# Performance work log

Measured on AMD Instinct MI355X. Metric: run time of the kernel, lower is better.

The kernel has to match this reference:

```python
import jax, jax.numpy as jnp
import numpy as np

D_MODEL = 512
N_HEAD = 8
D_HEAD = 64
N_LAYER = 4
D_INNER = 2048
IN_CH = 2048
N_CLS = 64
B, T = 2, 2048
LN_EPS = 1e-5


def layer_norm(x, s, b):
    mu = jnp.mean(x, axis=-1, keepdims=True)
    var = jnp.mean(jnp.square(x - mu), axis=-1, keepdims=True)
    return (x - mu) * jax.lax.rsqrt(var + LN_EPS) * s + b


def rel_shift(x):
    # x: [q, k, b, n] -> Transformer-XL relative shift
    q, k, b, n = x.shape
    zp = jnp.zeros((q, 1, b, n), x.dtype)
    x = jnp.concatenate([zp, x], axis=1)          # [q, k+1, b, n]
    x = x.reshape(k + 1, q, b, n)[1:]             # drop first row
    return x.reshape(q, k, b, n)


def setup_inputs() -> dict:
    key = jax.random.key(0)
    ks = jax.random.split(key, 12)
    s = 0.02
    return {
        "x": jax.random.normal(ks[0], (B, IN_CH, T), jnp.float32),
        "emb_w": jax.random.normal(ks[1], (D_MODEL, IN_CH), jnp.float32) * s,
        "emb_b": jnp.zeros((D_MODEL,), jnp.float32),
        "r_w_bias": jax.random.normal(ks[2], (N_HEAD, D_HEAD), jnp.float32) * s,
        "r_r_bias": jax.random.normal(ks[3], (N_HEAD, D_HEAD), jnp.float32) * s,
        "qkv_w": jax.random.normal(ks[4], (N_LAYER, 3 * N_HEAD * D_HEAD, D_MODEL), jnp.float32) * s,
        "qkv_b": jnp.zeros((N_LAYER, 3 * N_HEAD * D_HEAD), jnp.float32),
        "r_proj_w": jax.random.normal(ks[5], (N_LAYER, N_HEAD * D_HEAD, D_MODEL), jnp.float32) * s,
        "o_w": jax.random.normal(ks[6], (N_LAYER, D_MODEL, N_HEAD * D_HEAD), jnp.float32) * s,
        "ln1_s": jnp.ones((N_LAYER, D_MODEL), jnp.float32),
        "ln1_b": jnp.zeros((N_LAYER, D_MODEL), jnp.float32),
        "ff1_w": jax.random.normal(ks[7], (N_LAYER, D_INNER, D_MODEL), jnp.float32) * s,
        "ff1_b": jnp.zeros((N_LAYER, D_INNER), jnp.float32),
        "ff2_w": jax.random.normal(ks[8], (N_LAYER, D_MODEL, D_INNER), jnp.float32) * s,
        "ff2_b": jnp.zeros((N_LAYER, D_MODEL), jnp.float32),
        "ln2_s": jnp.ones((N_LAYER, D_MODEL), jnp.float32),
        "ln2_b": jnp.zeros((N_LAYER, D_MODEL), jnp.float32),
        "cls_w": jax.random.normal(ks[9], (N_CLS, D_MODEL), jnp.float32) * s,
        "cls_b": jnp.zeros((N_CLS,), jnp.float32),
    }


def reference(x, emb_w, emb_b, r_w_bias, r_r_bias, qkv_w, qkv_b, r_proj_w, o_w,
              ln1_s, ln1_b, ff1_w, ff1_b, ff2_w, ff2_b, ln2_s, ln2_b, cls_w, cls_b):
    b, _, t = x.shape
    d = D_MODEL
    # 1x1 conv embedding, then to [T, B, d_model] layout as in _forward
    h = jnp.einsum('dc,bct->tbd', emb_w, x) + emb_b

    # sinusoidal positional embedding over pos_seq = klen-1 .. 0 (klen == qlen, mem_len=0)
    pos_seq = jnp.arange(t - 1, -1, -1, dtype=h.dtype)
    inv_freq = 1.0 / (10000.0 ** (jnp.arange(0, d, 2, dtype=h.dtype) / d))
    sinusoid = pos_seq[:, None] * inv_freq[None, :]
    pos_emb = jnp.concatenate([jnp.sin(sinusoid), jnp.cos(sinusoid)], axis=-1)  # [T, d]

    scale = 1.0 / (D_HEAD ** 0.5)
    for i in range(N_LAYER):
        w = h
        heads = jnp.einsum('ed,tbd->tbe', qkv_w[i], w) + qkv_b[i]          # [T,B,3*H*Dh]
        q, k, v = jnp.split(heads, 3, axis=-1)
        q = q.reshape(t, b, N_HEAD, D_HEAD)
        k = k.reshape(t, b, N_HEAD, D_HEAD)
        v = v.reshape(t, b, N_HEAD, D_HEAD)
        r_head_k = jnp.einsum('ed,td->te', r_proj_w[i], pos_emb).reshape(t, N_HEAD, D_HEAD)

        AC = jnp.einsum('ibnd,jbnd->ijbn', q + r_w_bias, k)                # content term
        BD = rel_shift(jnp.einsum('ibnd,jnd->ijbn', q + r_r_bias, r_head_k))  # position term
        attn_prob = jax.nn.softmax((AC + BD) * scale, axis=1)              # softmax over keys
        attn_vec = jnp.einsum('ijbn,jbnd->ibnd', attn_prob, v).reshape(t, b, N_HEAD * D_HEAD)
        attn_out = jnp.einsum('de,tbe->tbd', o_w[i], attn_vec)             # o_net (no bias)
        h = layer_norm(w + attn_out, ln1_s[i], ln1_b[i])                   # post-lnorm

        ff = jnp.einsum('fd,tbd->tbf', ff1_w[i], h) + ff1_b[i]
        ff = jax.nn.relu(ff)
        ff = jnp.einsum('df,tbf->tbd', ff2_w[i], ff) + ff2_b[i]
        h = layer_norm(h + ff, ln2_s[i], ln2_b[i])

    # 1x1 conv classifier -> [B, num_classes, T]
    out = jnp.einsum('kd,tbd->bkt', cls_w, h) + cls_b[None, :, None]
    return out
```

## Files before the change

kernel.cpp:

```cpp
#include <hip/hip_runtime.h>
#include <hip/hip_bf16.h>
#include <math.h>


#define T_   2048
#define B_   2
#define DM   512
#define NH   8
#define DH   64
#define DI   2048
#define INCH 2048
#define NCLS 64
#define MT   4096

typedef __attribute__((ext_vector_type(8))) short short8;
typedef __attribute__((ext_vector_type(4))) float float4v;

#define QSCALE 0.1803368801111204f

__device__ inline ushort f2bf(float f) {
  uint u = __float_as_uint(f);
  return (ushort)((u + 0x7FFFu + ((u >> 16) & 1u)) >> 16);
}
__device__ inline float bf2f(ushort h) { return __uint_as_float(((uint)h) << 16); }
__device__ inline uint pkbf(float a, float b) {
  __hip_bfloat162 h = __float22bfloat162_rn(float2{a, b});
  return *(uint*)&h;
}
__device__ inline void gload16(const void* g, void* lds) {
  __builtin_amdgcn_global_load_lds(
      (const __attribute__((address_space(1))) void*)g,
      (__attribute__((address_space(3))) void*)lds, 16, 0, 0);
}

__global__ __launch_bounds__(256) void pos_kernel(ushort* __restrict__ pe) {
  int idx = blockIdx.x * 256 + threadIdx.x;
  if (idx >= T_ * DM) return;
  int t = idx >> 9;
  int i = idx & 511;
  int j = (i < 256) ? i : (i - 256);
  float invf = __builtin_amdgcn_exp2f((float)(-2 * j) * 0.025952563241307517f);
  float a = (float)(T_ - 1 - t) * invf;
  pe[idx] = f2bf((i < 256) ? sinf(a) : cosf(a));
}

__global__ __launch_bounds__(256) void cvt6_kernel(
    const float* s0, ushort* d0, int n0,
    const float* s1, ushort* d1, int n1,
    const float* s2, ushort* d2, int n2,
    const float* s3, ushort* d3, int n3,
    const float* s4, ushort* d4, int n4,
    const float* s5, ushort* d5, int n5)
{
  const float* s; ushort* d; int n;
  switch (blockIdx.y) {
    case 0: s = s0; d = d0; n = n0; break;
    case 1: s = s1; d = d1; n = n1; break;
    case 2: s = s2; d = d2; n = n2; break;
    case 3: s = s3; d = d3; n = n3; break;
    case 4: s = s4; d = d4; n = n4; break;
    default: s = s5; d = d5; n = n5; break;
  }
  int i = blockIdx.x * 256 + threadIdx.x;
  if (i >= n) return;
  float4 v = ((const float4*)s)[i];
  ushort4 w = { f2bf(v.x), f2bf(v.y), f2bf(v.z), f2bf(v.w) };
  ((ushort4*)d)[i] = w;
}

__global__ __launch_bounds__(256) void clsw_cvt_kernel(const float* __restrict__ w,
                                                       ushort* __restrict__ wb) {
  int i = blockIdx.x * 256 + threadIdx.x;
  ushort4 o;
  if (i < 8192) {
    float4 v = ((const float4*)w)[i];
    o = ushort4{ f2bf(v.x), f2bf(v.y), f2bf(v.z), f2bf(v.w) };
  } else {
    o = ushort4{ 0, 0, 0, 0 };
  }
  ((ushort4*)wb)[i] = o;
}

__global__ __launch_bounds__(256) void xpose_kernel(const float* __restrict__ x,
                                                    ushort* __restrict__ xb) {
  __shared__ float s[32][33];
  int t0 = blockIdx.x * 32, k0 = blockIdx.y * 32, b = blockIdx.z;
  int tx = threadIdx.x & 31, ty = threadIdx.x >> 5;
#pragma unroll
  for (int l = 0; l < 4; ++l) {
    int k = k0 + ty + l * 8;
    s[ty + l * 8][tx] = x[((size_t)b * INCH + k) * T_ + t0 + tx];
  }
  __syncthreads();
#pragma unroll
  for (int l = 0; l < 4; ++l) {
    int t = t0 + ty + l * 8;
    xb[((size_t)(t * 2 + b)) * INCH + k0 + tx] = f2bf(s[tx][ty + l * 8]);
  }
}

template<int TM, int OUTMODE, bool RELU>
__global__ __launch_bounds__(256) void gemm_bf16(
    const ushort* __restrict__ A, const ushort* __restrict__ W,
    const float* __restrict__ bias, float* __restrict__ Cf, ushort* __restrict__ Cb,
    int M, int N, int K)
{
  __shared__ __attribute__((aligned(16))) ushort As[TM * 64];
  __shared__ __attribute__((aligned(16))) ushort Bs[128 * 64];
  const int NI = TM / 32;
  const int tid  = threadIdx.x;
  const int wave = tid >> 6, lane = tid & 63;
  const int quad = lane >> 4, lidx = lane & 15;
  const int m0 = blockIdx.y * TM, n0 = blockIdx.x * 128;
  const int r8 = lane >> 3;
  const int cs = ((lane & 7) ^ (r8 & 7)) * 8;

  float4v acc[NI * 4];
#pragma unroll
  for (int i = 0; i < NI * 4; ++i) acc[i] = (float4v){0.f, 0.f, 0.f, 0.f};

  const int wm = (wave >> 1) * (TM / 2), wn = (wave & 1) * 64;

  for (int k0 = 0; k0 < K; k0 += 64) {
    __syncthreads();
#pragma unroll
    for (int g = 0; g < TM / 32; ++g) {
      int r0 = wave * 8 + g * 32;
      gload16(A + (size_t)(m0 + r0 + r8) * K + k0 + cs, &As[r0 * 64]);
    }
#pragma unroll
    for (int g = 0; g < 4; ++g) {
      int r0 = wave * 8 + g * 32;
      gload16(W + (size_t)(n0 + r0 + r8) * K + k0 + cs, &Bs[r0 * 64]);
    }
    __syncthreads();

#pragma unroll
    for (int kb = 0; kb < 2; ++kb) {
      short8 af[NI], bf4[4];
      const int ch = (((kb * 4 + quad) ^ (lidx & 7)) * 8);
#pragma unroll
      for (int i = 0; i < NI; ++i)
        af[i] = *(const short8*)&As[(wm + i * 16 + lidx) * 64 + ch];
#pragma unroll
      for (int j = 0; j < 4; ++j)
        bf4[j] = *(const short8*)&Bs[(wn + j * 16 + lidx) * 64 + ch];
#pragma unroll
      for (int i = 0; i < NI; ++i)
#pragma unroll
        for (int j = 0; j < 4; ++j)
          acc[i * 4 + j] = __builtin_amdgcn_mfma_f32_16x16x32_bf16(af[i], bf4[j], acc[i * 4 + j], 0, 0, 0);
    }
  }

  float bj[4];
#pragma unroll
  for (int j = 0; j < 4; ++j) bj[j] = bias ? bias[n0 + wn + j * 16 + lidx] : 0.f;

  if (OUTMODE == 3 && n0 >= 1024) {
    ushort* vt = (ushort*)Cf;
    __syncthreads();
#pragma unroll
    for (int i = 0; i < NI; ++i)
#pragma unroll
      for (int j = 0; j < 4; ++j)
#pragma unroll
        for (int reg = 0; reg < 4; ++reg) {
          int c2 = wn + j * 16 + lidx;
          int rl = wm + i * 16 + quad * 4 + reg;
          float v = acc[i * 4 + j][reg] + bj[j];
          ushort* buf = (c2 < 64) ? As : Bs;
          buf[(c2 & 63) * 128 + (rl ^ ((c2 & 7) << 4))] = f2bf(v);
        }
    __syncthreads();
    const int t0g = m0 >> 1;
    const int low = tid & 15, b2 = low & 1, tb = low >> 1;
#pragma unroll
    for (int s = 0; s < 8; ++s) {
      int dd = s * 16 + (tid >> 4);
      const ushort* buf = (dd < 64) ? As : Bs;
      ushort tmp[8];
#pragma unroll
      for (int q2 = 0; q2 < 8; ++q2) {
        int rl = (tb * 8 + q2) * 2 + b2;
        tmp[q2] = buf[(dd & 63) * 128 + (rl ^ ((dd & 7) << 4))];
      }
      int dg = n0 + dd - 1024;
      int n2h = dg >> 6, ddd = dg & 63;
      *(uint4*)&vt[((size_t)((b2 * 8 + n2h) * 64 + ddd)) * (size_t)T_ + t0g + tb * 8] = *(uint4*)tmp;
    }
  } else {
#pragma unroll
    for (int i = 0; i < NI; ++i) {
      int rbase = m0 + wm + i * 16 + quad * 4;
#pragma unroll
      for (int j = 0; j < 4; ++j) {
        int col = n0 + wn + j * 16 + lidx;
#pragma unroll
        for (int reg = 0; reg < 4; ++reg) {
          float v = acc[i * 4 + j][reg] + bj[j];
          if (RELU) v = fmaxf(v, 0.f);
          size_t off = (size_t)(rbase + reg) * N + col;
          if (OUTMODE == 0 || OUTMODE == 2) Cf[off] = v;
          if (OUTMODE != 0) Cb[off] = f2bf(v);
        }
      }
    }
  }
}

#define GT 68

__device__ inline short8 bfrag(const char* base, int lidx, int quad, int kb) {
  return *(const short8*)(base + lidx * 128 + ((((kb << 2) + quad) ^ (lidx & 7)) << 4));
}

__global__ __launch_bounds__(256, 3) void attn_mfma_kernel(
    const ushort* __restrict__ heads, const ushort* __restrict__ rk,
    const ushort* __restrict__ vtg,
    const float* __restrict__ rwb, const float* __restrict__ rrb,
    float* __restrict__ O0, float* __restrict__ O1, float* __restrict__ O2,
    float* __restrict__ Lp)
{
  __shared__ __attribute__((aligned(16))) ushort Ks[64 * 64];
  __shared__ __attribute__((aligned(16))) ushort Vt[64 * 64];
  __shared__ __attribute__((aligned(16))) ushort Re[128 * 64];
  __shared__ __attribute__((aligned(16))) ushort Gbt[128 * GT];

  const int tid  = threadIdx.x;
  const int F = blockIdx.x + ((blockIdx.y + (blockIdx.z << 4)) << 5);
  const int g  = F & 7;
  const int k  = F >> 3;
  const int r  = k / 96;
  const int kk = k - r * 96;
  const int bnl = r * 8 + g;
  const int i0   = (kk & 31) * 64;
  const int chunk = kk >> 5;
  const int b    = bnl & 1;
  const int n    = bnl >> 1;
  const int jt0 = (chunk == 0) ? 0  : (chunk == 1 ? 11 : 22);
  const int jt1 = (chunk == 0) ? 11 : (chunk == 1 ? 22 : 32);
  const int wave = tid >> 6;
  const int lane = tid & 63;
  const int quad = lane >> 4;
  const int lidx = lane & 15;
  const int r8   = lane >> 3;
  const int cs8  = ((lane & 7) ^ (r8 & 7)) * 8;
  const int bn64 = (b * 8 + n) * 64;
  const int rloc = wave * 16 + lidx;

  short8 qw[2], qr4[4][2], q4[2];
  {
    auto qfrag = [&](int row, int kb, const float* bias) -> short8 {
      short8 q;
      if (row < T_) q = *(const short8*)&heads[(size_t)(row * 2 + b) * 1536 + n * 64 + kb * 32 + quad * 8];
      else { for (int t = 0; t < 8; ++t) ((ushort*)&q)[t] = 0; }
      short8 o;
#pragma unroll
      for (int t = 0; t < 8; ++t) {
        float f = (bf2f((ushort)((ushort*)&q)[t]) + bias[n * 64 + kb * 32 + quad * 8 + t]) * QSCALE;
        ((ushort*)&o)[t] = f2bf(f);
      }
      return o;
    };
    qw[0] = qfrag(i0 + rloc, 0, rwb);
    qw[1] = qfrag(i0 + rloc, 1, rwb);
#pragma unroll
    for (int rt = 0; rt < 4; ++rt) {
      int row = i0 + rt * 16 + lidx;
      qr4[rt][0] = qfrag(row, 0, rrb); qr4[rt][1] = qfrag(row, 1, rrb);
    }
    int row4 = i0 + 64 + lidx;
    q4[0] = qfrag(row4, 0, rrb); q4[1] = qfrag(row4, 1, rrb);
  }

  int a0[4];
#pragma unroll
  for (int t = 0; t < 4; ++t)
    a0[t] = (t * 16 + quad * 4 + 63 - rloc) * GT + rloc;

  float4v oacc[4];
  float4v liacc = (float4v){0.f, 0.f, 0.f, 0.f};
#pragma unroll
  for (int dt = 0; dt < 4; ++dt) oacc[dt] = (float4v){0.f, 0.f, 0.f, 0.f};
  short8 ones8;
#pragma unroll
  for (int t = 0; t < 8; ++t) ((ushort*)&ones8)[t] = 0x3F80;

  auto stageK = [&](int jt) {
    int j0 = jt * 64;
#pragma unroll
    for (int half = 0; half < 2; ++half) {
      int r0 = 8 * wave + 32 * half;
      gload16(heads + (size_t)((j0 + r0 + r8) * 2 + b) * 1536 + 512 + n * 64 + cs8, &Ks[r0 * 64]);
    }
  };
  auto stageReFull = [&](int jt) {
    int qmin = jt * 64 + 1984 - i0;
#pragma unroll
    for (int q4i = 0; q4i < 4; ++q4i) {
      int r0 = 8 * wave + 32 * q4i;
      int qh = qmin + r0 + r8;
      int p  = (qh > T_) ? (qh - T_ - 1) : ((qh == T_) ? 0 : qh);
      gload16(rk + (size_t)p * 2048 + n * 64 + cs8, &Re[r0 * 64]);
    }
  };
  auto stageReNew = [&](int jt, int roff) {
    int qmin = jt * 64 + 1984 - i0;
#pragma unroll
    for (int half = 0; half < 2; ++half) {
      int u0 = 8 * wave + 32 * half;
      int qh = qmin + 128 + u0 + r8;
      int p  = (qh > T_) ? (qh - T_ - 1) : ((qh == T_) ? 0 : qh);
      gload16(rk + (size_t)p * 2048 + n * 64 + cs8, &Re[(u0 + roff) * 64]);
    }
  };
  auto stageV = [&](int jt) {
    int j0 = jt * 64;
#pragma unroll
    for (int half = 0; half < 2; ++half) {
      int r0 = 8 * wave + 32 * half;
      gload16(vtg + (size_t)(bn64 + r0 + r8) * (size_t)T_ + j0 + cs8, &Vt[r0 * 64]);
    }
  };

  stageK(jt0);
  stageReFull(jt0);
  stageV(jt0);
  __syncthreads();
  {
    int Tidx = T_ - (jt0 * 64 + 1984 - i0);
    if (Tidx >= 0 && Tidx < 128) {
      if (tid < 32) ((uint*)Re)[Tidx * 32 + tid] = 0u;
      __syncthreads();
    }
  }

  int roff = 0;

  for (int jt = jt0; jt < jt1; ++jt) {
    const int qmin = jt * 64 + 1984 - i0;
    const int wth  = T_ - qmin;

    float4v sv[4];
#pragma unroll
    for (int t = 0; t < 4; ++t) {
      const char* KsT = (const char*)Ks + t * 2048;
      short8 kf0 = bfrag(KsT, lidx, quad, 0);
      short8 kf1 = bfrag(KsT, lidx, quad, 1);
      float4v c = {0.f, 0.f, 0.f, 0.f};
      c = __builtin_amdgcn_mfma_f32_16x16x32_bf16(kf0, qw[0], c, 0, 0, 0);
      c = __builtin_amdgcn_mfma_f32_16x16x32_bf16(kf1, qw[1], c, 0, 0, 0);
      sv[t] = c;
    }

#pragma unroll
    for (int si = 0; si < 2; ++si) {
      const int ws = wave + si * 4;
      const int w0 = ws * 16;
      const char* ReW = (const char*)Re + (size_t)(((w0 + roff) & 127) * 128);
      short8 rb0 = bfrag(ReW, lidx, quad, 0);
      short8 rb1 = bfrag(ReW, lidx, quad, 1);
#pragma unroll
      for (int rt = 0; rt < 4; ++rt) {
        bool need = si == 0 ? (rt >= 3 - wave) : (rt <= 3 - wave);
        if (need) {
          float4v g2 = {0.f, 0.f, 0.f, 0.f};
          g2 = __builtin_amdgcn_mfma_f32_16x16x32_bf16(qr4[rt][0], rb0, g2, 0, 0, 0);
          g2 = __builtin_amdgcn_mfma_f32_16x16x32_bf16(qr4[rt][1], rb1, g2, 0, 0, 0);
          uint2 st; st.x = pkbf(g2[0], g2[1]); st.y = pkbf(g2[2], g2[3]);
          *(uint2*)&Gbt[(w0 + lidx) * GT + rt * 16 + quad * 4] = st;
        }
      }
      if (si == 0 && wth < 63) {
        float4v g2 = {0.f, 0.f, 0.f, 0.f};
        g2 = __builtin_amdgcn_mfma_f32_16x16x32_bf16(q4[0], rb0, g2, 0, 0, 0);
        g2 = __builtin_amdgcn_mfma_f32_16x16x32_bf16(q4[1], rb1, g2, 0, 0, 0);
        if (quad == 0) Gbt[(w0 + lidx) * GT + 64] = f2bf(g2[0]);
      }
    }
    __syncthreads();

    if (jt + 1 < jt1) {
      stageK(jt + 1);
      stageReNew(jt, roff);
    }

    if (wth >= 126) {
#pragma unroll
      for (int t = 0; t < 4; ++t)
#pragma unroll
        for (int r2 = 0; r2 < 4; ++r2)
          sv[t][r2] = __builtin_amdgcn_exp2f(sv[t][r2] + bf2f(Gbt[a0[t] + r2 * GT]));
    } else if (wth < 0) {
#pragma unroll
      for (int t = 0; t < 4; ++t)
#pragma unroll
        for (int r2 = 0; r2 < 4; ++r2)
          sv[t][r2] = __builtin_amdgcn_exp2f(sv[t][r2] + bf2f(Gbt[a0[t] + r2 * GT + 1]));
    } else {
      const int cth = wth + rloc - 63;
#pragma unroll
      for (int t = 0; t < 4; ++t) {
        const int c0 = t * 16 + quad * 4;
#pragma unroll
        for (int r2 = 0; r2 < 4; ++r2) {
          int ga = a0[t] + r2 * GT + ((c0 + r2 > cth) ? 1 : 0);
          sv[t][r2] = __builtin_amdgcn_exp2f(sv[t][r2] + bf2f(Gbt[ga]));
        }
      }
    }

    short8 vb[4][2];
#pragma unroll
    for (int dt = 0; dt < 4; ++dt) {
      const char* VtT = (const char*)Vt + dt * 2048;
      vb[dt][0] = bfrag(VtT, lidx, quad, 0);
      vb[dt][1] = bfrag(VtT, lidx, quad, 1);
    }

    short8 af[2];
#pragma unroll
    for (int kb = 0; kb < 2; ++kb) {
      uint mm[4];
#pragma unroll
      for (int i = 0; i < 2; ++i) {
        uint e, o;
        asm("v_cvt_pk_bf16_f32 %0, %1, %2" : "=v"(e) : "v"(sv[2 * kb][2 * i]),     "v"(sv[2 * kb][2 * i + 1]));
        asm("v_cvt_pk_bf16_f32 %0, %1, %2" : "=v"(o) : "v"(sv[2 * kb + 1][2 * i]), "v"(sv[2 * kb + 1][2 * i + 1]));
        asm("v_permlane32_swap_b32 %0, %1" : "+v"(e), "+v"(o));
        asm("v_permlane16_swap_b32 %0, %1" : "+v"(e), "+v"(o));
        mm[i] = e; mm[2 + i] = o;
      }
      union { uint u[4]; short8 s; } cv;
      cv.u[0] = mm[0]; cv.u[1] = mm[1]; cv.u[2] = mm[2]; cv.u[3] = mm[3];
      af[kb] = cv.s;
    }

#pragma unroll
    for (int dt = 0; dt < 4; ++dt) {
      oacc[dt] = __builtin_amdgcn_mfma_f32_16x16x32_bf16(af[0], vb[dt][0], oacc[dt], 0, 0, 0);
      oacc[dt] = __builtin_amdgcn_mfma_f32_16x16x32_bf16(af[1], vb[dt][1], oacc[dt], 0, 0, 0);
    }
    liacc = __builtin_amdgcn_mfma_f32_16x16x32_bf16(af[0], ones8, liacc, 0, 0, 0);
    liacc = __builtin_amdgcn_mfma_f32_16x16x32_bf16(af[1], ones8, liacc, 0, 0, 0);

    __syncthreads();

    if (jt + 1 < jt1) {
      stageV(jt + 1);
      roff ^= 64;
      {
        int Tn = T_ - ((jt + 1) * 64 + 1984 - i0);
        if (Tn >= 64 && Tn < 128) {
          int phys = (Tn + roff) & 127;
          if (tid < 32) ((uint*)Re)[phys * 32 + tid] = 0u;
          __syncthreads();
        }
      }
    }
  }

  float* __restrict__ Oc = (chunk == 0) ? O0 : (chunk == 1 ? O1 : O2);
  float* __restrict__ Lc = Lp + chunk * (16 * T_);
  const int rowg0 = (b * 8 + n) * T_ + i0 + wave * 16 + quad * 4;
#pragma unroll
  for (int reg = 0; reg < 4; ++reg) {
    int rowg = rowg0 + reg;
#pragma unroll
    for (int dt = 0; dt < 4; ++dt)
      Oc[(size_t)rowg * 64 + dt * 16 + lidx] = oacc[dt][reg];
    if (lidx == 0) Lc[rowg] = liacc[reg];
  }
}

__global__ __launch_bounds__(256) void attn_norm_kernel(
    const float* __restrict__ O0, const float* __restrict__ O1,
    const float* __restrict__ O2, const float* __restrict__ Lp,
    ushort* __restrict__ avec)
{
  int idx = blockIdx.x * 256 + threadIdx.x;
  int d4  = idx & 15;
  int row = (idx >> 4) & 2047;
  int bn  = idx >> 15;
  float4 v0 = ((const float4*)O0)[idx];
  float4 v1 = ((const float4*)O1)[idx];
  float4 v2 = ((const float4*)O2)[idx];
  int rg = (bn << 11) + row;
  float li = Lp[rg] + Lp[rg + 16 * T_] + Lp[rg + 32 * T_];
  float inv = 1.0f / li;
  int b = bn >> 3, n = bn & 7;
  ushort4 w = { f2bf((v0.x + v1.x + v2.x) * inv), f2bf((v0.y + v1.y + v2.y) * inv),
                f2bf((v0.z + v1.z + v2.z) * inv), f2bf((v0.w + v1.w + v2.w) * inv) };
  *(ushort4*)&avec[(size_t)(row * 2 + b) * DM + n * 64 + d4 * 4] = w;
}

__global__ __launch_bounds__(256) void ln_res_kernel(
    float* __restrict__ h, ushort* __restrict__ hb, const float* __restrict__ delta,
    const float* __restrict__ s, const float* __restrict__ bb)
{
  const int m = blockIdx.x;
  const int tid = threadIdx.x;
  float* hp = h + (size_t)m * DM;
  ushort* hbp = hb + (size_t)m * DM;
  const float* dp = delta + (size_t)m * DM;
  float x0 = hp[tid] + dp[tid];
  float x1 = hp[tid + 256] + dp[tid + 256];
  float sum = x0 + x1, sq = x0 * x0 + x1 * x1;
#pragma unroll
  for (int o = 32; o > 0; o >>= 1) { sum += __shfl_down(sum, o); sq += __shfl_down(sq, o); }
  __shared__ float part[8];
  int wv = tid >> 6;
  if ((tid & 63) == 0) { part[wv * 2] = sum; part[wv * 2 + 1] = sq; }
  __syncthreads();
  float ts = part[0] + part[2] + part[4] + part[6];
  float tq = part[1] + part[3] + part[5] + part[7];
  float mu = ts * (1.f / DM);
  float var = tq * (1.f / DM) - mu * mu;
  float rs = rsqrtf(var + 1e-5f);
  float y0 = (x0 - mu) * rs * s[tid]       + bb[tid];
  float y1 = (x1 - mu) * rs * s[tid + 256] + bb[tid + 256];
  hp[tid] = y0;       hbp[tid] = f2bf(y0);
  hp[tid + 256] = y1; hbp[tid + 256] = f2bf(y1);
}

__global__ __launch_bounds__(256) void reorder_kernel(const float* __restrict__ ct,
                                                      const float* __restrict__ cb,
                                                      float* __restrict__ out) {
  int idx = blockIdx.x * 256 + threadIdx.x;
  if (idx >= B_ * NCLS * T_) return;
  int t  = idx & (T_ - 1);
  int nc = (idx >> 11) & 63;
  int bb = idx >> 17;
  out[idx] = ct[(size_t)(t * B_ + bb) * 128 + nc] + cb[nc];
}

extern "C" void kernel_launch(void* const* d_in, const int* in_sizes, int n_in,
                              void* d_out, int out_size, void* d_ws, size_t ws_size,
                              hipStream_t stream)
{
  const float* x     = (const float*)d_in[0];
  const float* emb_w = (const float*)d_in[1];
  const float* emb_b = (const float*)d_in[2];
  const float* rwb   = (const float*)d_in[3];
  const float* rrb   = (const float*)d_in[4];
  const float* qkv_w = (const float*)d_in[5];
  const float* qkv_b = (const float*)d_in[6];
  const float* rproj = (const float*)d_in[7];
  const float* o_w   = (const float*)d_in[8];
  const float* ln1s  = (const float*)d_in[9];
  const float* ln1b  = (const float*)d_in[10];
  const float* ff1w  = (const float*)d_in[11];
  const float* ff1b  = (const float*)d_in[12];
  const float* ff2w  = (const float*)d_in[13];
  const float* ff2b  = (const float*)d_in[14];
  const float* ln2s  = (const float*)d_in[15];
  const float* ln2b  = (const float*)d_in[16];
  const float* clsw  = (const float*)d_in[17];
  const float* clsb  = (const float*)d_in[18];
  float* out = (float*)d_out;

  char* p = (char*)d_ws;
  float*  h       = (float*)p;   p += (size_t)MT * DM * 4;
  float*  tmpf    = (float*)p;   p += (size_t)MT * DM * 4;
  ushort* hb      = (ushort*)p;  p += (size_t)MT * DM * 2;
  ushort* headsb  = (ushort*)p;  p += (size_t)MT * 1536 * 2;
  ushort* peb     = (ushort*)p;  p += (size_t)T_ * DM * 2;
  ushort* rk_all  = (ushort*)p;  p += (size_t)T_ * 2048 * 2;
  ushort* avecb   = (ushort*)p;  p += (size_t)MT * DM * 2;
  ushort* xfb     = (ushort*)p;  p += (size_t)MT * INCH * 2;
  ushort* emb_wb  = (ushort*)p;  p += (size_t)DM * INCH * 2;
  ushort* qkv_wb  = (ushort*)p;  p += (size_t)4 * 1536 * DM * 2;
  ushort* rproj_wb= (ushort*)p;  p += (size_t)4 * DM * DM * 2;
  ushort* o_wb    = (ushort*)p;  p += (size_t)4 * DM * DM * 2;
  ushort* ff1_wb  = (ushort*)p;  p += (size_t)4 * DI * DM * 2;
  ushort* ff2_wb  = (ushort*)p;  p += (size_t)4 * DM * DI * 2;
  float*  P2      = (float*)p;   p += (size_t)MT * DM * 4;
  float*  Lp      = (float*)p;   p += (size_t)3 * 16 * T_ * 4;
  ushort* cls_wb  = (ushort*)p;  p += (size_t)128 * DM * 2;
  ushort* vtg     = xfb;
  float*  P0      = tmpf;
  float*  P1      = (float*)(xfb + (size_t)16 * 64 * T_);

  cvt6_kernel<<<dim3(4096, 6), 256, 0, stream>>>(
      emb_w, emb_wb, DM * INCH / 4,
      qkv_w, qkv_wb, 4 * 1536 * DM / 4,
      rproj, rproj_wb, 4 * DM * DM / 4,
      o_w,   o_wb,   4 * DM * DM / 4,
      ff1w,  ff1_wb, 4 * DI * DM / 4,
      ff2w,  ff2_wb, 4 * DM * DI / 4);
  clsw_cvt_kernel<<<64, 256, 0, stream>>>(clsw, cls_wb);
  pos_kernel<<<(T_ * DM) / 256, 256, 0, stream>>>(peb);
  xpose_kernel<<<dim3(T_ / 32, INCH / 32, B_), 256, 0, stream>>>(x, xfb);

  gemm_bf16<64, 2, false><<<dim3(DM / 128, MT / 64), 256, 0, stream>>>(
      xfb, emb_wb, emb_b, h, hb, MT, DM, INCH);
  gemm_bf16<128, 1, false><<<dim3(2048 / 128, T_ / 128), 256, 0, stream>>>(
      peb, rproj_wb, nullptr, nullptr, rk_all, T_, 2048, DM);

  for (int l = 0; l < 4; ++l) {
    gemm_bf16<128, 3, false><<<dim3(1536 / 128, MT / 128), 256, 0, stream>>>(
        hb, qkv_wb + (size_t)l * 1536 * DM, qkv_b + l * 1536, (float*)vtg, headsb, MT, 1536, DM);
    attn_mfma_kernel<<<dim3(T_ / 64, B_ * NH, 3), 256, 0, stream>>>(
        headsb, rk_all + (size_t)l * 512, vtg, rwb, rrb, P0, P1, P2, Lp);
    attn_norm_kernel<<<(16 * T_ * 16) / 256, 256, 0, stream>>>(P0, P1, P2, Lp, avecb);
    gemm_bf16<32, 0, false><<<dim3(DM / 128, MT / 32), 256, 0, stream>>>(
        avecb, o_wb + (size_t)l * DM * DM, nullptr, tmpf, nullptr, MT, DM, DM);
    ln_res_kernel<<<MT, 256, 0, stream>>>(h, hb, tmpf, ln1s + l * DM, ln1b + l * DM);
    gemm_bf16<128, 1, true><<<dim3(DI / 128, MT / 128), 256, 0, stream>>>(
        hb, ff1_wb + (size_t)l * DI * DM, ff1b + l * DI, nullptr, xfb, MT, DI, DM);
    gemm_bf16<32, 0, false><<<dim3(DM / 128, MT / 32), 256, 0, stream>>>(
        xfb, ff2_wb + (size_t)l * DM * DI, ff2b + l * DM, tmpf, nullptr, MT, DM, DI);
    ln_res_kernel<<<MT, 256, 0, stream>>>(h, hb, tmpf, ln2s + l * DM, ln2b + l * DM);
  }

  gemm_bf16<32, 0, false><<<dim3(1, MT / 32), 256, 0, stream>>>(
      hb, cls_wb, nullptr, tmpf, nullptr, MT, 128, DM);
  reorder_kernel<<<(B_ * NCLS * T_) / 256, 256, 0, stream>>>(tmpf, clsb, out);
}
```

Before: 809.2 us.

## Emit K and V in MFMA fragment layout from QKV GEMM, drop attention LDS staging

The QKV GEMM epilogue now writes K and V tiles straight into a pre-swizzled per-lane MFMA fragment layout in global memory. The attention kernel then loads its K and V operands directly into registers with 16-byte vector loads and no longer stages them through shared memory. Removing the Ks and Vt shared buffers lowers LDS use, so launch bounds rise from 3 to 4 blocks per CU. The tradeoff is that these loads are not overlapped with compute the way the old staging was, so global-load latency is more exposed, and the GEMM epilogue for K becomes more complex.

```diff
diff --git a/kernel.cpp b/kernel.cpp
--- a/kernel.cpp
+++ b/kernel.cpp
@@ -103,7 +103,7 @@
 __global__ __launch_bounds__(256) void gemm_bf16(
     const ushort* __restrict__ A, const ushort* __restrict__ W,
     const float* __restrict__ bias, float* __restrict__ Cf, ushort* __restrict__ Cb,
-    int M, int N, int K)
+    int M, int N, int K, ushort* __restrict__ Kf, ushort* __restrict__ Vf)
 {
   __shared__ __attribute__((aligned(16))) ushort As[TM * 64];
   __shared__ __attribute__((aligned(16))) ushort Bs[128 * 64];
@@ -157,8 +157,11 @@
 #pragma unroll
   for (int j = 0; j < 4; ++j) bj[j] = bias ? bias[n0 + wn + j * 16 + lidx] : 0.f;
 
-  if (OUTMODE == 3 && n0 >= 1024) {
-    ushort* vt = (ushort*)Cf;
+  if (OUTMODE == 3 && n0 >= 512) {
+    const bool isV = (n0 >= 1024);
+    ushort* frag = isV ? Vf : Kf;
+    const int hbase = (isV ? (n0 - 1024) : (n0 - 512)) >> 6;
+    const int jt = m0 >> 7;
     __syncthreads();
 #pragma unroll
     for (int i = 0; i < NI; ++i)
@@ -173,21 +176,34 @@
           buf[(c2 & 63) * 128 + (rl ^ ((c2 & 7) << 4))] = f2bf(v);
         }
     __syncthreads();
-    const int t0g = m0 >> 1;
-    const int low = tid & 15, b2 = low & 1, tb = low >> 1;
 #pragma unroll
     for (int s = 0; s < 8; ++s) {
-      int dd = s * 16 + (tid >> 4);
-      const ushort* buf = (dd < 64) ? As : Bs;
+      int eid = tid + s * 256;
+      int lane2 = eid & 63;
+      int kbf = (eid >> 6) & 1, tf = (eid >> 7) & 3, hh = (eid >> 9) & 1, bb2 = eid >> 10;
+      int quadf = lane2 >> 4, lidxf = lane2 & 15;
       ushort tmp[8];
-#pragma unroll
-      for (int q2 = 0; q2 < 8; ++q2) {
-        int rl = (tb * 8 + q2) * 2 + b2;
-        tmp[q2] = buf[(dd & 63) * 128 + (rl ^ ((dd & 7) << 4))];
-      }
-      int dg = n0 + dd - 1024;
-      int n2h = dg >> 6, ddd = dg & 63;
-      *(uint4*)&vt[((size_t)((b2 * 8 + n2h) * 64 + ddd)) * (size_t)T_ + t0g + tb * 8] = *(uint4*)tmp;
+      if (isV) {
+        int c2 = hh * 64 + tf * 16 + lidxf;
+        const ushort* buf = (c2 < 64) ? As : Bs;
+        int rowb = (c2 & 63) * 128, sw = (c2 & 7) << 4;
+#pragma unroll
+        for (int jj = 0; jj < 8; ++jj) {
+          int rl = (kbf * 32 + quadf * 8 + jj) * 2 + bb2;
+          tmp[jj] = buf[rowb + (rl ^ sw)];
+        }
+      } else {
+        int rl = (tf * 16 + lidxf) * 2 + bb2;
+#pragma unroll
+        for (int jj = 0; jj < 8; ++jj) {
+          int c2 = hh * 64 + kbf * 32 + quadf * 8 + jj;
+          const ushort* buf = (c2 < 64) ? As : Bs;
+          tmp[jj] = buf[(c2 & 63) * 128 + (rl ^ ((c2 & 7) << 4))];
+        }
+      }
+      int bn2 = bb2 * 8 + hbase + hh;
+      ushort* dst = frag + ((((size_t)bn2 * 32 + jt) * 4 + tf) * 2 + kbf) * 512 + lane2 * 8;
+      *(uint4*)dst = *(uint4*)tmp;
     }
   } else {
 #pragma unroll
@@ -215,15 +231,13 @@
   return *(const short8*)(base + lidx * 128 + ((((kb << 2) + quad) ^ (lidx & 7)) << 4));
 }
 
-__global__ __launch_bounds__(256, 3) void attn_mfma_kernel(
+__global__ __launch_bounds__(256, 4) void attn_mfma_kernel(
     const ushort* __restrict__ heads, const ushort* __restrict__ rk,
-    const ushort* __restrict__ vtg,
+    const ushort* __restrict__ kfg, const ushort* __restrict__ vfg,
     const float* __restrict__ rwb, const float* __restrict__ rrb,
     float* __restrict__ O0, float* __restrict__ O1, float* __restrict__ O2,
     float* __restrict__ Lp)
 {
-  __shared__ __attribute__((aligned(16))) ushort Ks[64 * 64];
-  __shared__ __attribute__((aligned(16))) ushort Vt[64 * 64];
   __shared__ __attribute__((aligned(16))) ushort Re[128 * 64];
   __shared__ __attribute__((aligned(16))) ushort Gbt[128 * GT];
 
@@ -246,7 +260,7 @@
   const int lidx = lane & 15;
   const int r8   = lane >> 3;
   const int cs8  = ((lane & 7) ^ (r8 & 7)) * 8;
-  const int bn64 = (b * 8 + n) * 64;
+  const int bn8  = b * 8 + n;
   const int rloc = wave * 16 + lidx;
 
   short8 qw[2], qr4[4][2], q4[2];
@@ -287,14 +301,6 @@
 #pragma unroll
   for (int t = 0; t < 8; ++t) ((ushort*)&ones8)[t] = 0x3F80;
 
-  auto stageK = [&](int jt) {
-    int j0 = jt * 64;
-#pragma unroll
-    for (int half = 0; half < 2; ++half) {
-      int r0 = 8 * wave + 32 * half;
-      gload16(heads + (size_t)((j0 + r0 + r8) * 2 + b) * 1536 + 512 + n * 64 + cs8, &Ks[r0 * 64]);
-    }
-  };
   auto stageReFull = [&](int jt) {
     int qmin = jt * 64 + 1984 - i0;
 #pragma unroll
@@ -315,18 +321,8 @@
       gload16(rk + (size_t)p * 2048 + n * 64 + cs8, &Re[(u0 + roff) * 64]);
     }
   };
-  auto stageV = [&](int jt) {
-    int j0 = jt * 64;
-#pragma unroll
-    for (int half = 0; half < 2; ++half) {
-      int r0 = 8 * wave + 32 * half;
-      gload16(vtg + (size_t)(bn64 + r0 + r8) * (size_t)T_ + j0 + cs8, &Vt[r0 * 64]);
-    }
-  };
-
-  stageK(jt0);
+
   stageReFull(jt0);
-  stageV(jt0);
   __syncthreads();
   {
     int Tidx = T_ - (jt0 * 64 + 1984 - i0);
@@ -342,15 +338,20 @@
     const int qmin = jt * 64 + 1984 - i0;
     const int wth  = T_ - qmin;
 
+    const ushort* kp = kfg + (((size_t)bn8 * 32 + jt) * 8) * 512 + lane * 8;
+    short8 kf[4][2];
+#pragma unroll
+    for (int t = 0; t < 4; ++t) {
+      kf[t][0] = *(const short8*)(kp + (t * 2 + 0) * 512);
+      kf[t][1] = *(const short8*)(kp + (t * 2 + 1) * 512);
+    }
+
     float4v sv[4];
 #pragma unroll
     for (int t = 0; t < 4; ++t) {
-      const char* KsT = (const char*)Ks + t * 2048;
-      short8 kf0 = bfrag(KsT, lidx, quad, 0);
-      short8 kf1 = bfrag(KsT, lidx, quad, 1);
       float4v c = {0.f, 0.f, 0.f, 0.f};
-      c = __builtin_amdgcn_mfma_f32_16x16x32_bf16(kf0, qw[0], c, 0, 0, 0);
-      c = __builtin_amdgcn_mfma_f32_16x16x32_bf16(kf1, qw[1], c, 0, 0, 0);
+      c = __builtin_amdgcn_mfma_f32_16x16x32_bf16(kf[t][0], qw[0], c, 0, 0, 0);
+      c = __builtin_amdgcn_mfma_f32_16x16x32_bf16(kf[t][1], qw[1], c, 0, 0, 0);
       sv[t] = c;
     }
 
@@ -381,9 +382,14 @@
     }
     __syncthreads();
 
-    if (jt + 1 < jt1) {
-      stageK(jt + 1);
-      stageReNew(jt, roff);
+    if (jt + 1 < jt1) stageReNew(jt, roff);
+
+    const ushort* vp = vfg + (((size_t)bn8 * 32 + jt) * 8) * 512 + lane * 8;
+    short8 vb[4][2];
+#pragma unroll
+    for (int dt = 0; dt < 4; ++dt) {
+      vb[dt][0] = *(const short8*)(vp + (dt * 2 + 0) * 512);
+      vb[dt][1] = *(const short8*)(vp + (dt * 2 + 1) * 512);
     }
 
     if (wth >= 126) {
@@ -409,14 +415,6 @@
           sv[t][r2] = __builtin_amdgcn_exp2f(sv[t][r2] + bf2f(Gbt[ga]));
         }
       }
-    }
-
-    short8 vb[4][2];
-#pragma unroll
-    for (int dt = 0; dt < 4; ++dt) {
-      const char* VtT = (const char*)Vt + dt * 2048;
-      vb[dt][0] = bfrag(VtT, lidx, quad, 0);
-      vb[dt][1] = bfrag(VtT, lidx, quad, 1);
     }
 
     short8 af[2];
@@ -448,7 +446,6 @@
     __syncthreads();
 
     if (jt + 1 < jt1) {
-      stageV(jt + 1);
       roff ^= 64;
       {
         int Tn = T_ - ((jt + 1) * 64 + 1984 - i0);
@@ -463,7 +460,7 @@
 
   float* __restrict__ Oc = (chunk == 0) ? O0 : (chunk == 1 ? O1 : O2);
   float* __restrict__ Lc = Lp + chunk * (16 * T_);
-  const int rowg0 = (b * 8 + n) * T_ + i0 + wave * 16 + quad * 4;
+  const int rowg0 = bn8 * T_ + i0 + wave * 16 + quad * 4;
 #pragma unroll
   for (int reg = 0; reg < 4; ++reg) {
     int rowg = rowg0 + reg;
@@ -578,9 +575,10 @@
   float*  P2      = (float*)p;   p += (size_t)MT * DM * 4;
   float*  Lp      = (float*)p;   p += (size_t)3 * 16 * T_ * 4;
   ushort* cls_wb  = (ushort*)p;  p += (size_t)128 * DM * 2;
-  ushort* vtg     = xfb;
+  ushort* kfg     = xfb;
+  float*  P1      = (float*)(xfb + (size_t)2 * 1024 * 1024);
+  ushort* vfg     = xfb + (size_t)6 * 1024 * 1024;
   float*  P0      = tmpf;
-  float*  P1      = (float*)(xfb + (size_t)16 * 64 * T_);
 
   cvt6_kernel<<<dim3(4096, 6), 256, 0, stream>>>(
       emb_w, emb_wb, DM * INCH / 4,
@@ -594,27 +592,28 @@
   xpose_kernel<<<dim3(T_ / 32, INCH / 32, B_), 256, 0, stream>>>(x, xfb);
 
   gemm_bf16<64, 2, false><<<dim3(DM / 128, MT / 64), 256, 0, stream>>>(
-      xfb, emb_wb, emb_b, h, hb, MT, DM, INCH);
+      xfb, emb_wb, emb_b, h, hb, MT, DM, INCH, nullptr, nullptr);
   gemm_bf16<128, 1, false><<<dim3(2048 / 128, T_ / 128), 256, 0, stream>>>(
-      peb, rproj_wb, nullptr, nullptr, rk_all, T_, 2048, DM);
+      peb, rproj_wb, nullptr, nullptr, rk_all, T_, 2048, DM, nullptr, nullptr);
 
   for (int l = 0; l < 4; ++l) {
     gemm_bf16<128, 3, false><<<dim3(1536 / 128, MT / 128), 256, 0, stream>>>(
-        hb, qkv_wb + (size_t)l * 1536 * DM, qkv_b + l * 1536, (float*)vtg, headsb, MT, 1536, DM);
+        hb, qkv_wb + (size_t)l * 1536 * DM, qkv_b + l * 1536, nullptr, headsb,
+        MT, 1536, DM, kfg, vfg);
     attn_mfma_kernel<<<dim3(T_ / 64, B_ * NH, 3), 256, 0, stream>>>(
-        headsb, rk_all + (size_t)l * 512, vtg, rwb, rrb, P0, P1, P2, Lp);
+        headsb, rk_all + (size_t)l * 512, kfg, vfg, rwb, rrb, P0, P1, P2, Lp);
     attn_norm_kernel<<<(16 * T_ * 16) / 256, 256, 0, stream>>>(P0, P1, P2, Lp, avecb);
     gemm_bf16<32, 0, false><<<dim3(DM / 128, MT / 32), 256, 0, stream>>>(
-        avecb, o_wb + (size_t)l * DM * DM, nullptr, tmpf, nullptr, MT, DM, DM);
+        avecb, o_wb + (size_t)l * DM * DM, nullptr, tmpf, nullptr, MT, DM, DM, nullptr, nullptr);
     ln_res_kernel<<<MT, 256, 0, stream>>>(h, hb, tmpf, ln1s + l * DM, ln1b + l * DM);
     gemm_bf16<128, 1, true><<<dim3(DI / 128, MT / 128), 256, 0, stream>>>(
-        hb, ff1_wb + (size_t)l * DI * DM, ff1b + l * DI, nullptr, xfb, MT, DI, DM);
+        hb, ff1_wb + (size_t)l * DI * DM, ff1b + l * DI, nullptr, xfb, MT, DI, DM, nullptr, nullptr);
     gemm_bf16<32, 0, false><<<dim3(DM / 128, MT / 32), 256, 0, stream>>>(
-        xfb, ff2_wb + (size_t)l * DM * DI, ff2b + l * DM, tmpf, nullptr, MT, DM, DI);
+        xfb, ff2_wb + (size_t)l * DM * DI, ff2b + l * DM, tmpf, nullptr, MT, DM, DI, nullptr, nullptr);
     ln_res_kernel<<<MT, 256, 0, stream>>>(h, hb, tmpf, ln2s + l * DM, ln2b + l * DM);
   }
 
   gemm_bf16<32, 0, false><<<dim3(1, MT / 32), 256, 0, stream>>>(
-      hb, cls_wb, nullptr, tmpf, nullptr, MT, 128, DM);
+      hb, cls_wb, nullptr, tmpf, nullptr, MT, 128, DM, nullptr, nullptr);
   reorder_kernel<<<(B_ * NCLS * T_) / 256, 256, 0, stream>>>(tmpf, clsb, out);
 }
```

Result: slower. 1.046 ms (+29.2%).
